# Performance work log

Hardware: AMD Instinct MI355X
Metric: run time of the kernel (lower is better)

Reference implementation:

```python
import jax, jax.numpy as jnp
import numpy as np

D_MODEL = 2048
HEADS = 16
HEAD_DIM = D_MODEL // HEADS
INNER = 8192
SEQ = 2048
EPS = 1e-5


def _layernorm(x, g, b):
    mu = jnp.mean(x, axis=-1, keepdims=True)
    var = jnp.mean(jnp.square(x - mu), axis=-1, keepdims=True)
    return (x - mu) * jax.lax.rsqrt(var + EPS) * g + b


def setup_inputs() -> dict:
    key = jax.random.key(0)
    ks = jax.random.split(key, 10)
    s = 0.02
    return {
        "x": jax.random.normal(ks[0], (1, SEQ, D_MODEL), dtype=jnp.float32),
        "C_w": jax.random.normal(ks[1], (D_MODEL, 3 * D_MODEL), dtype=jnp.float32) * s,
        "C_b": jnp.zeros((3 * D_MODEL,), dtype=jnp.float32),
        "lin_w": jax.random.normal(ks[2], (D_MODEL, D_MODEL), dtype=jnp.float32) * s,
        "lin_b": jnp.zeros((D_MODEL,), dtype=jnp.float32),
        "ff1_w": jax.random.normal(ks[3], (D_MODEL, INNER), dtype=jnp.float32) * s,
        "ff1_b": jnp.zeros((INNER,), dtype=jnp.float32),
        "ff2_w": jax.random.normal(ks[4], (INNER, D_MODEL), dtype=jnp.float32) * s,
        "ff2_b": jnp.zeros((D_MODEL,), dtype=jnp.float32),
        "ln1_g": jnp.ones((D_MODEL,), dtype=jnp.float32),
        "ln1_b": jnp.zeros((D_MODEL,), dtype=jnp.float32),
        "ln2_g": jnp.ones((D_MODEL,), dtype=jnp.float32),
        "ln2_b": jnp.zeros((D_MODEL,), dtype=jnp.float32),
    }


def reference(x, C_w, C_b, lin_w, lin_b, ff1_w, ff1_b, ff2_w, ff2_b,
              ln1_g, ln1_b, ln2_g, ln2_b):
    b, s, d = x.shape
    c = x @ C_w + C_b                       # [b, s, 3d]
    q, k, v = jnp.split(c, 3, axis=2)
    q = q.reshape(b, s, HEADS, HEAD_DIM)
    k = k.reshape(b, s, HEADS, HEAD_DIM)
    v = v.reshape(b, s, HEADS, HEAD_DIM)
    # NOTE: source scales by sqrt(d_model), NOT sqrt(head_dim)
    qk = jnp.einsum('bqhd,bkhd->bhqk', q, k) / jnp.sqrt(jnp.float32(d))
    causal = jnp.tril(jnp.ones((s, s), dtype=bool))  # [s, s]
    qk = jnp.where(causal[None, None, :, :], qk, -jnp.inf)
    scores = jax.nn.softmax(qk, axis=3)
    out = jnp.einsum('bhqk,bkhd->bqhd', scores, v).reshape(b, s, d)
    attn = out @ lin_w + lin_b
    h1 = _layernorm(x + attn, ln1_g, ln1_b)
    ff = jax.nn.gelu(h1 @ ff1_w + ff1_b, approximate=False) @ ff2_w + ff2_b
    return _layernorm(h1 + ff, ln2_g, ln2_b)
```

## Files before the change

kernel.cpp:

```cpp
#include <hip/hip_runtime.h>
#include <hip/hip_bf16.h>

#define SEQ 2048
#define DM 2048
#define NH 16
#define HD 128
#define FF 8192

typedef float f4v __attribute__((ext_vector_type(4)));
typedef short s8v __attribute__((ext_vector_type(8)));

__device__ __forceinline__ ushort f2bf(float f) {
  unsigned int x = __float_as_uint(f);
  unsigned int r = (x + 0x7FFFu + ((x >> 16) & 1u)) >> 16;
  return (ushort)r;
}

#define AS1 __attribute__((address_space(1)))
#define AS3 __attribute__((address_space(3)))
__device__ __forceinline__ void load16_lds(const ushort* g, ushort* l) {
  __builtin_amdgcn_global_load_lds((const AS1 unsigned int*)g, (AS3 unsigned int*)l, 16, 0, 0);
}

__global__ __launch_bounds__(256) void k_cvt(const float* __restrict__ in,
                                             ushort* __restrict__ out, int n4) {
  int i = blockIdx.x * 256 + threadIdx.x;
  if (i >= n4) return;
  f4v v = reinterpret_cast<const f4v*>(in)[i];
  ushort4 u;
  u.x = f2bf(v[0]); u.y = f2bf(v[1]); u.z = f2bf(v[2]); u.w = f2bf(v[3]);
  reinterpret_cast<ushort4*>(out)[i] = u;
}

__global__ __launch_bounds__(256) void k_tr(const float* __restrict__ W,
                                            ushort* __restrict__ Wt,
                                            int K, int N) {
  __shared__ float tile[32][36];
  int t = threadIdx.x;
  int n0 = blockIdx.x * 32, k0 = blockIdx.y * 32;
  int lr = t >> 3, lc = (t & 7) * 4;
  *(f4v*)&tile[lr][lc] = *(const f4v*)&W[(size_t)(k0 + lr) * N + n0 + lc];
  __syncthreads();
  int sn = t >> 3, sk = (t & 7) * 4;
  ushort4 u;
  u.x = f2bf(tile[sk + 0][sn]);
  u.y = f2bf(tile[sk + 1][sn]);
  u.z = f2bf(tile[sk + 2][sn]);
  u.w = f2bf(tile[sk + 3][sn]);
  *(ushort4*)&Wt[(size_t)(n0 + sn) * K + k0 + sk] = u;
}

#define GBM 256
#define GBN 256
#define GBK 32
#define TILE_SH (GBM * GBK)

__global__ __launch_bounds__(512, 2) void k_gemm256(
    const ushort* __restrict__ A, const ushort* __restrict__ Bt,
    const float* __restrict__ bias, float* __restrict__ Cf,
    ushort* __restrict__ Cb, int M, int N, int K, int gelu) {
  __shared__ ushort As[4 * TILE_SH];
  __shared__ ushort Bs[4 * TILE_SH];
  const int m0 = blockIdx.y * GBM, n0 = blockIdx.x * GBN;
  const int t = threadIdx.x;
  const int w = t >> 6, lane = t & 63;
  const int quad = lane >> 4, l16 = lane & 15;
  const int wm = (w >> 2) * 128, wn = (w & 3) * 64;
  const int kchunk = K / gridDim.z;
  const int kbeg = blockIdx.z * kchunk;
  const int NT = kchunk / GBK;
  if (Cf && gridDim.z > 1) Cf += (size_t)blockIdx.z * M * N;

  const int srow = lane >> 2;
  const int cg = (lane & 3) ^ ((srow >> 1) & 3);
  const ushort* gA = A + (size_t)(m0 + w * 32 + srow) * K + kbeg + cg * 8;
  const ushort* gB = Bt + (size_t)(n0 + w * 32 + srow) * K + kbeg + cg * 8;
  const int swz = (quad ^ ((l16 >> 1) & 3)) * 8;
  const int baseA = (wm + l16) * GBK + swz;
  const int baseB = (wn + l16) * GBK + swz;

  f4v acc[8][4] = {};

#pragma unroll
  for (int pt = 0; pt < 3; ++pt) {
    ushort* lA = &As[pt * TILE_SH + (w * 32) * GBK];
    ushort* lB = &Bs[pt * TILE_SH + (w * 32) * GBK];
    load16_lds(gA + pt * GBK, lA);
    load16_lds(gA + pt * GBK + (size_t)16 * K, lA + 16 * GBK);
    load16_lds(gB + pt * GBK, lB);
    load16_lds(gB + pt * GBK + (size_t)16 * K, lB + 16 * GBK);
  }
  asm volatile("s_waitcnt vmcnt(8)\n\ts_barrier" ::: "memory");

  for (int tt = 0; tt < NT; ++tt) {
    const ushort* At = &As[(tt & 3) * TILE_SH];
    const ushort* Bc = &Bs[(tt & 3) * TILE_SH];
    const int nb = (tt + 3) & 3;
    s8v a[8], b0, b1;
#pragma unroll
    for (int i = 0; i < 8; ++i)
      a[i] = *(const s8v*)&At[baseA + i * 16 * GBK];
    b0 = *(const s8v*)&Bc[baseB + 0 * 16 * GBK];
    b1 = *(const s8v*)&Bc[baseB + 1 * 16 * GBK];
    if (tt + 3 < NT) {
      ushort* lA = &As[nb * TILE_SH + (w * 32) * GBK];
      load16_lds(gA + (size_t)(tt + 3) * GBK, lA);
      load16_lds(gA + (size_t)(tt + 3) * GBK + (size_t)16 * K, lA + 16 * GBK);
    }
    __builtin_amdgcn_s_setprio(1);
#pragma unroll
    for (int i = 0; i < 8; ++i) {
      acc[i][0] = __builtin_amdgcn_mfma_f32_16x16x32_bf16(a[i], b0, acc[i][0], 0, 0, 0);
      acc[i][1] = __builtin_amdgcn_mfma_f32_16x16x32_bf16(a[i], b1, acc[i][1], 0, 0, 0);
    }
    __builtin_amdgcn_s_setprio(0);
    asm volatile("s_barrier" ::: "memory");
    s8v b2 = *(const s8v*)&Bc[baseB + 2 * 16 * GBK];
    s8v b3 = *(const s8v*)&Bc[baseB + 3 * 16 * GBK];
    if (tt + 3 < NT) {
      ushort* lB = &Bs[nb * TILE_SH + (w * 32) * GBK];
      load16_lds(gB + (size_t)(tt + 3) * GBK, lB);
      load16_lds(gB + (size_t)(tt + 3) * GBK + (size_t)16 * K, lB + 16 * GBK);
    }
    __builtin_amdgcn_s_setprio(1);
#pragma unroll
    for (int i = 0; i < 8; ++i) {
      acc[i][2] = __builtin_amdgcn_mfma_f32_16x16x32_bf16(a[i], b2, acc[i][2], 0, 0, 0);
      acc[i][3] = __builtin_amdgcn_mfma_f32_16x16x32_bf16(a[i], b3, acc[i][3], 0, 0, 0);
    }
    __builtin_amdgcn_s_setprio(0);
    if (tt + 4 <= NT) {
      asm volatile("s_waitcnt vmcnt(8)\n\ts_barrier" ::: "memory");
    } else if (tt + 3 <= NT) {
      asm volatile("s_waitcnt vmcnt(4)\n\ts_barrier" ::: "memory");
    } else if (tt + 2 <= NT) {
      asm volatile("s_waitcnt vmcnt(0)\n\ts_barrier" ::: "memory");
    }
  }

#pragma unroll
  for (int i = 0; i < 8; ++i) {
    int rbase = m0 + wm + i * 16 + quad * 4;
#pragma unroll
    for (int j = 0; j < 4; ++j) {
      int cidx = n0 + wn + j * 16 + l16;
      float b = bias ? bias[cidx] : 0.0f;
#pragma unroll
      for (int r = 0; r < 4; ++r) {
        float v = acc[i][j][r] + b;
        if (gelu) v = 0.5f * v * (1.0f + erff(v * 0.70710678118654752f));
        if (Cf) Cf[(size_t)(rbase + r) * N + cidx] = v;
        if (Cb) Cb[(size_t)(rbase + r) * N + cidx] = f2bf(v);
      }
    }
  }
}

__global__ __launch_bounds__(256) void k_attn_mfma(const ushort* __restrict__ qkv,
                                                   ushort* __restrict__ ctx) {
  __shared__ ushort Ks[64][136];
  __shared__ ushort Vt[128][72];
  __shared__ ushort Ps[4][16][72];
  const int idx = blockIdx.x;
  const int h = idx & (NH - 1);
  const int qt = (SEQ / 64 - 1) - (idx >> 4);
  const int q0 = qt * 64;
  const int t = threadIdx.x;
  const int wave = t >> 6, lane = t & 63;
  const int quad = lane >> 4, l16 = lane & 15;
  const float scale = 0.022097086912079608f;

  s8v aq[4];
  {
    const ushort* qp = qkv + (size_t)(q0 + 16 * wave + l16) * (3 * DM) + h * HD + quad * 8;
#pragma unroll
    for (int ks = 0; ks < 4; ++ks)
      aq[ks] = *(const s8v*)(qp + ks * 32);
  }
  f4v acc_o[8] = {};
  float m_r[4], l_r[4];
#pragma unroll
  for (int r = 0; r < 4; ++r) { m_r[r] = -1e30f; l_r[r] = 0.0f; }

  for (int kt = 0; kt <= qt; ++kt) {
    const int k0 = kt * 64;
    __syncthreads();
    {
      const ushort* kp = qkv + (size_t)k0 * (3 * DM) + DM + h * HD;
#pragma unroll
      for (int i = 0; i < 4; ++i) {
        int ch = t + i * 256;
        int row = ch >> 4, c8 = (ch & 15) * 8;
        *(s8v*)&Ks[row][c8] = *(const s8v*)(kp + (size_t)row * (3 * DM) + c8);
      }
      const ushort* vp = qkv + (size_t)k0 * (3 * DM) + 2 * DM + h * HD;
#pragma unroll
      for (int i = 0; i < 4; ++i) {
        int id = t + i * 256;
        int d = id & 127, sg = id >> 7;
        ushort e0 = vp[(size_t)(sg * 8 + 0) * (3 * DM) + d];
        ushort e1 = vp[(size_t)(sg * 8 + 1) * (3 * DM) + d];
        ushort e2 = vp[(size_t)(sg * 8 + 2) * (3 * DM) + d];
        ushort e3 = vp[(size_t)(sg * 8 + 3) * (3 * DM) + d];
        ushort e4 = vp[(size_t)(sg * 8 + 4) * (3 * DM) + d];
        ushort e5 = vp[(size_t)(sg * 8 + 5) * (3 * DM) + d];
        ushort e6 = vp[(size_t)(sg * 8 + 6) * (3 * DM) + d];
        ushort e7 = vp[(size_t)(sg * 8 + 7) * (3 * DM) + d];
        uint4 pk;
        pk.x = (uint)e0 | ((uint)e1 << 16);
        pk.y = (uint)e2 | ((uint)e3 << 16);
        pk.z = (uint)e4 | ((uint)e5 << 16);
        pk.w = (uint)e6 | ((uint)e7 << 16);
        *(uint4*)&Vt[d][sg * 8] = pk;
      }
    }
    __syncthreads();

    f4v sacc[4] = {};
#pragma unroll
    for (int ks = 0; ks < 4; ++ks) {
      s8v bk[4];
#pragma unroll
      for (int j = 0; j < 4; ++j)
        bk[j] = *(const s8v*)&Ks[j * 16 + l16][ks * 32 + quad * 8];
#pragma unroll
      for (int j = 0; j < 4; ++j)
        sacc[j] = __builtin_amdgcn_mfma_f32_16x16x32_bf16(aq[ks], bk[j], sacc[j], 0, 0, 0);
    }
    if (kt == qt) {
#pragma unroll
      for (int j = 0; j < 4; ++j)
#pragma unroll
        for (int r = 0; r < 4; ++r) {
          int lrow = 16 * wave + quad * 4 + r;
          int lcol = j * 16 + l16;
          sacc[j][r] = (lcol > lrow) ? -1e30f : sacc[j][r] * scale;
        }
    } else {
#pragma unroll
      for (int j = 0; j < 4; ++j)
#pragma unroll
        for (int r = 0; r < 4; ++r) sacc[j][r] *= scale;
    }
    float alpha[4];
#pragma unroll
    for (int r = 0; r < 4; ++r) {
      float mx = fmaxf(fmaxf(sacc[0][r], sacc[1][r]), fmaxf(sacc[2][r], sacc[3][r]));
      mx = fmaxf(mx, __shfl_xor(mx, 1));
      mx = fmaxf(mx, __shfl_xor(mx, 2));
      mx = fmaxf(mx, __shfl_xor(mx, 4));
      mx = fmaxf(mx, __shfl_xor(mx, 8));
      float mn = fmaxf(m_r[r], mx);
      alpha[r] = __expf(m_r[r] - mn);
      m_r[r] = mn;
      float ps = 0.0f;
#pragma unroll
      for (int j = 0; j < 4; ++j) {
        float p = __expf(sacc[j][r] - mn);
        sacc[j][r] = p;
        ps += p;
      }
      ps += __shfl_xor(ps, 1);
      ps += __shfl_xor(ps, 2);
      ps += __shfl_xor(ps, 4);
      ps += __shfl_xor(ps, 8);
      l_r[r] = l_r[r] * alpha[r] + ps;
    }
#pragma unroll
    for (int j = 0; j < 4; ++j)
#pragma unroll
      for (int r = 0; r < 4; ++r)
        Ps[wave][quad * 4 + r][j * 16 + l16] = f2bf(sacc[j][r]);
#pragma unroll
    for (int nd = 0; nd < 8; ++nd)
#pragma unroll
      for (int r = 0; r < 4; ++r) acc_o[nd][r] *= alpha[r];
#pragma unroll
    for (int ks2 = 0; ks2 < 2; ++ks2) {
      s8v ap = *(const s8v*)&Ps[wave][l16][ks2 * 32 + quad * 8];
#pragma unroll
      for (int nd = 0; nd < 8; ++nd) {
        s8v bv = *(const s8v*)&Vt[nd * 16 + l16][ks2 * 32 + quad * 8];
        acc_o[nd] = __builtin_amdgcn_mfma_f32_16x16x32_bf16(ap, bv, acc_o[nd], 0, 0, 0);
      }
    }
  }
  float rl[4];
#pragma unroll
  for (int r = 0; r < 4; ++r) rl[r] = 1.0f / l_r[r];
#pragma unroll
  for (int nd = 0; nd < 8; ++nd) {
    int col = h * HD + nd * 16 + l16;
#pragma unroll
    for (int r = 0; r < 4; ++r) {
      int row = q0 + 16 * wave + quad * 4 + r;
      ctx[(size_t)row * DM + col] = f2bf(acc_o[nd][r] * rl[r]);
    }
  }
}

__global__ __launch_bounds__(256) void k_ln_sk(const float* __restrict__ A,
                                               const float* __restrict__ P, int np,
                                               const float* __restrict__ bias,
                                               const float* __restrict__ g,
                                               const float* __restrict__ be,
                                               float* __restrict__ outf,
                                               ushort* __restrict__ outb) {
  int row = blockIdx.x;
  int t = threadIdx.x;
  const f4v* av = reinterpret_cast<const f4v*>(A + (size_t)row * DM);
  f4v x0 = av[t];
  f4v x1 = av[t + 256];
  for (int s = 0; s < np; ++s) {
    const f4v* pv = reinterpret_cast<const f4v*>(P + (size_t)s * SEQ * DM + (size_t)row * DM);
    x0 += pv[t];
    x1 += pv[t + 256];
  }
  const f4v* bb = reinterpret_cast<const f4v*>(bias);
  x0 += bb[t];
  x1 += bb[t + 256];
  float s = x0[0] + x0[1] + x0[2] + x0[3] + x1[0] + x1[1] + x1[2] + x1[3];
  float q = x0[0]*x0[0] + x0[1]*x0[1] + x0[2]*x0[2] + x0[3]*x0[3]
          + x1[0]*x1[0] + x1[1]*x1[1] + x1[2]*x1[2] + x1[3]*x1[3];
#pragma unroll
  for (int off = 32; off; off >>= 1) {
    s += __shfl_down(s, off, 64);
    q += __shfl_down(q, off, 64);
  }
  __shared__ float rs[4], rq[4];
  if ((t & 63) == 0) { rs[t >> 6] = s; rq[t >> 6] = q; }
  __syncthreads();
  s = rs[0] + rs[1] + rs[2] + rs[3];
  q = rq[0] + rq[1] + rq[2] + rq[3];
  float mu = s * (1.0f / DM);
  float var = q * (1.0f / DM) - mu * mu;
  float rstd = rsqrtf(var + 1e-5f);
  const f4v* gv = reinterpret_cast<const f4v*>(g);
  const f4v* bev = reinterpret_cast<const f4v*>(be);
  f4v y0 = (x0 - mu) * rstd * gv[t] + bev[t];
  f4v y1 = (x1 - mu) * rstd * gv[t + 256] + bev[t + 256];
  reinterpret_cast<f4v*>(outf + (size_t)row * DM)[t] = y0;
  reinterpret_cast<f4v*>(outf + (size_t)row * DM)[t + 256] = y1;
  if (outb) {
    ushort4 u0, u1;
    u0.x = f2bf(y0[0]); u0.y = f2bf(y0[1]); u0.z = f2bf(y0[2]); u0.w = f2bf(y0[3]);
    u1.x = f2bf(y1[0]); u1.y = f2bf(y1[1]); u1.z = f2bf(y1[2]); u1.w = f2bf(y1[3]);
    reinterpret_cast<ushort4*>(outb + (size_t)row * DM)[t] = u0;
    reinterpret_cast<ushort4*>(outb + (size_t)row * DM)[t + 256] = u1;
  }
}

extern "C" void kernel_launch(void* const* d_in, const int* in_sizes, int n_in,
                              void* d_out, int out_size, void* d_ws, size_t ws_size,
                              hipStream_t stream) {
  const float* x     = (const float*)d_in[0];
  const float* C_w   = (const float*)d_in[1];
  const float* C_b   = (const float*)d_in[2];
  const float* lin_w = (const float*)d_in[3];
  const float* lin_b = (const float*)d_in[4];
  const float* ff1_w = (const float*)d_in[5];
  const float* ff1_b = (const float*)d_in[6];
  const float* ff2_w = (const float*)d_in[7];
  const float* ff2_b = (const float*)d_in[8];
  const float* ln1g  = (const float*)d_in[9];
  const float* ln1b  = (const float*)d_in[10];
  const float* ln2g  = (const float*)d_in[11];
  const float* ln2b  = (const float*)d_in[12];

  char* ws = (char*)d_ws;
  size_t off = 0;
  auto take = [&](size_t bytes) {
    char* p = ws + off;
    off += (bytes + 255) & ~(size_t)255;
    return p;
  };
  ushort* Wt   = (ushort*)take((size_t)FF * DM * 2);
  ushort* qkvb = (ushort*)take((size_t)SEQ * 3 * DM * 2);
  ushort* xb   = (ushort*)take((size_t)SEQ * DM * 2);
  ushort* ctxb = (ushort*)take((size_t)SEQ * DM * 2);
  ushort* bigb = (ushort*)take((size_t)SEQ * FF * 2);
  float*  h1   = (float*) take((size_t)SEQ * DM * 4);
  float*  part = (float*) take((size_t)4 * SEQ * DM * 4);

  k_cvt<<<SEQ * DM / 1024, 256, 0, stream>>>(x, xb, SEQ * DM / 4);
  k_tr<<<dim3(3 * DM / 32, DM / 32), 256, 0, stream>>>(C_w, Wt, DM, 3 * DM);
  k_gemm256<<<dim3(3 * DM / 256, SEQ / 256, 1), 512, 0, stream>>>(xb, Wt, C_b, nullptr, qkvb, SEQ, 3 * DM, DM, 0);
  k_attn_mfma<<<dim3((SEQ / 64) * NH), 256, 0, stream>>>(qkvb, ctxb);
  k_tr<<<dim3(DM / 32, DM / 32), 256, 0, stream>>>(lin_w, Wt, DM, DM);
  k_gemm256<<<dim3(DM / 256, SEQ / 256, 4), 512, 0, stream>>>(ctxb, Wt, nullptr, part, nullptr, SEQ, DM, DM, 0);
  k_ln_sk<<<SEQ, 256, 0, stream>>>(x, part, 4, lin_b, ln1g, ln1b, h1, xb);
  k_tr<<<dim3(FF / 32, DM / 32), 256, 0, stream>>>(ff1_w, Wt, DM, FF);
  k_gemm256<<<dim3(FF / 256, SEQ / 256, 1), 512, 0, stream>>>(xb, Wt, ff1_b, nullptr, bigb, SEQ, FF, DM, 1);
  k_tr<<<dim3(DM / 32, FF / 32), 256, 0, stream>>>(ff2_w, Wt, FF, DM);
  k_gemm256<<<dim3(DM / 256, SEQ / 256, 4), 512, 0, stream>>>(bigb, Wt, nullptr, part, nullptr, SEQ, DM, FF, 0);
  k_ln_sk<<<SEQ, 256, 0, stream>>>(h1, part, 4, ff2_b, ln2g, ln2b, (float*)d_out, (ushort*)nullptr);
}
```

Measured before the change: 609.1 us.

## Split GEMM loop into four phases with register-prefetched LDS fragments

Restructures the bf16 MFMA GEMM main loop into four quarter-tile phases. While the current tile's MFMAs run, the A and B fragments for the next phase, and for the next k-tile, are loaded from LDS into registers. The global-to-LDS loads and their wait-count handling are interleaved across the phases. The aim is to hide LDS read latency behind matrix-core work. In exchange it doubles the number of barriers per iteration and adds more fragment registers, which could reduce occupancy or add synchronisation stalls.

```diff
diff --git a/kernel.cpp b/kernel.cpp
--- a/kernel.cpp
+++ b/kernel.cpp
@@ -21,6 +21,8 @@
 __device__ __forceinline__ void load16_lds(const ushort* g, ushort* l) {
   __builtin_amdgcn_global_load_lds((const AS1 unsigned int*)g, (AS3 unsigned int*)l, 16, 0, 0);
 }
+
+#define MFMA16(a, b, c) __builtin_amdgcn_mfma_f32_16x16x32_bf16((a), (b), (c), 0, 0, 0)
 
 __global__ __launch_bounds__(256) void k_cvt(const float* __restrict__ in,
                                              ushort* __restrict__ out, int n4) {
@@ -80,6 +82,7 @@
   const int baseB = (wn + l16) * GBK + swz;
 
   f4v acc[8][4] = {};
+  s8v A0[4], A1[4], B01[2], B23[2];
 
 #pragma unroll
   for (int pt = 0; pt < 3; ++pt) {
@@ -90,52 +93,82 @@
     load16_lds(gB + pt * GBK, lB);
     load16_lds(gB + pt * GBK + (size_t)16 * K, lB + 16 * GBK);
   }
-  asm volatile("s_waitcnt vmcnt(8)\n\ts_barrier" ::: "memory");
+  asm volatile("s_waitcnt vmcnt(8)" ::: "memory");
+  asm volatile("s_barrier" ::: "memory");
+#pragma unroll
+  for (int i = 0; i < 4; ++i) A0[i] = *(const s8v*)&As[baseA + i * 16 * GBK];
+  B01[0] = *(const s8v*)&Bs[baseB + 0 * 16 * GBK];
+  B01[1] = *(const s8v*)&Bs[baseB + 1 * 16 * GBK];
 
   for (int tt = 0; tt < NT; ++tt) {
-    const ushort* At = &As[(tt & 3) * TILE_SH];
-    const ushort* Bc = &Bs[(tt & 3) * TILE_SH];
-    const int nb = (tt + 3) & 3;
-    s8v a[8], b0, b1;
-#pragma unroll
-    for (int i = 0; i < 8; ++i)
-      a[i] = *(const s8v*)&At[baseA + i * 16 * GBK];
-    b0 = *(const s8v*)&Bc[baseB + 0 * 16 * GBK];
-    b1 = *(const s8v*)&Bc[baseB + 1 * 16 * GBK];
-    if (tt + 3 < NT) {
-      ushort* lA = &As[nb * TILE_SH + (w * 32) * GBK];
-      load16_lds(gA + (size_t)(tt + 3) * GBK, lA);
-      load16_lds(gA + (size_t)(tt + 3) * GBK + (size_t)16 * K, lA + 16 * GBK);
-    }
+    const ushort* Atc = &As[(tt & 3) * TILE_SH];
+    const ushort* Btc = &Bs[(tt & 3) * TILE_SH];
+    const ushort* Atn = &As[((tt + 1) & 3) * TILE_SH];
+    const ushort* Btn = &Bs[((tt + 1) & 3) * TILE_SH];
+    ushort* sA = &As[((tt + 3) & 3) * TILE_SH + (w * 32) * GBK];
+    ushort* sB = &Bs[((tt + 3) & 3) * TILE_SH + (w * 32) * GBK];
+    const bool st = (tt + 3 < NT), nx = (tt + 1 < NT);
+
+    B23[0] = *(const s8v*)&Btc[baseB + 2 * 16 * GBK];
+    B23[1] = *(const s8v*)&Btc[baseB + 3 * 16 * GBK];
+    if (st) {
+      load16_lds(gA + (size_t)(tt + 3) * GBK, sA);
+      load16_lds(gA + (size_t)(tt + 3) * GBK + (size_t)16 * K, sA + 16 * GBK);
+    }
+    asm volatile("s_barrier" ::: "memory");
     __builtin_amdgcn_s_setprio(1);
 #pragma unroll
-    for (int i = 0; i < 8; ++i) {
-      acc[i][0] = __builtin_amdgcn_mfma_f32_16x16x32_bf16(a[i], b0, acc[i][0], 0, 0, 0);
-      acc[i][1] = __builtin_amdgcn_mfma_f32_16x16x32_bf16(a[i], b1, acc[i][1], 0, 0, 0);
+    for (int i = 0; i < 4; ++i) {
+      acc[i][0] = MFMA16(A0[i], B01[0], acc[i][0]);
+      acc[i][1] = MFMA16(A0[i], B01[1], acc[i][1]);
     }
     __builtin_amdgcn_s_setprio(0);
+
+#pragma unroll
+    for (int i = 0; i < 4; ++i) A1[i] = *(const s8v*)&Atc[baseA + (i + 4) * 16 * GBK];
+    if (st) {
+      load16_lds(gB + (size_t)(tt + 3) * GBK, sB);
+      load16_lds(gB + (size_t)(tt + 3) * GBK + (size_t)16 * K, sB + 16 * GBK);
+      asm volatile("s_waitcnt vmcnt(8)" ::: "memory");
+    } else if (tt + 2 < NT) {
+      asm volatile("s_waitcnt vmcnt(4)" ::: "memory");
+    } else if (tt + 1 < NT) {
+      asm volatile("s_waitcnt vmcnt(0)" ::: "memory");
+    }
     asm volatile("s_barrier" ::: "memory");
-    s8v b2 = *(const s8v*)&Bc[baseB + 2 * 16 * GBK];
-    s8v b3 = *(const s8v*)&Bc[baseB + 3 * 16 * GBK];
-    if (tt + 3 < NT) {
-      ushort* lB = &Bs[nb * TILE_SH + (w * 32) * GBK];
-      load16_lds(gB + (size_t)(tt + 3) * GBK, lB);
-      load16_lds(gB + (size_t)(tt + 3) * GBK + (size_t)16 * K, lB + 16 * GBK);
-    }
     __builtin_amdgcn_s_setprio(1);
 #pragma unroll
-    for (int i = 0; i < 8; ++i) {
-      acc[i][2] = __builtin_amdgcn_mfma_f32_16x16x32_bf16(a[i], b2, acc[i][2], 0, 0, 0);
-      acc[i][3] = __builtin_amdgcn_mfma_f32_16x16x32_bf16(a[i], b3, acc[i][3], 0, 0, 0);
+    for (int i = 0; i < 4; ++i) {
+      acc[i][2] = MFMA16(A0[i], B23[0], acc[i][2]);
+      acc[i][3] = MFMA16(A0[i], B23[1], acc[i][3]);
     }
     __builtin_amdgcn_s_setprio(0);
-    if (tt + 4 <= NT) {
-      asm volatile("s_waitcnt vmcnt(8)\n\ts_barrier" ::: "memory");
-    } else if (tt + 3 <= NT) {
-      asm volatile("s_waitcnt vmcnt(4)\n\ts_barrier" ::: "memory");
-    } else if (tt + 2 <= NT) {
-      asm volatile("s_waitcnt vmcnt(0)\n\ts_barrier" ::: "memory");
-    }
+
+    if (nx) {
+#pragma unroll
+      for (int i = 0; i < 4; ++i) A0[i] = *(const s8v*)&Atn[baseA + i * 16 * GBK];
+    }
+    asm volatile("s_barrier" ::: "memory");
+    __builtin_amdgcn_s_setprio(1);
+#pragma unroll
+    for (int i = 0; i < 4; ++i) {
+      acc[i + 4][0] = MFMA16(A1[i], B01[0], acc[i + 4][0]);
+      acc[i + 4][1] = MFMA16(A1[i], B01[1], acc[i + 4][1]);
+    }
+    __builtin_amdgcn_s_setprio(0);
+
+    if (nx) {
+      B01[0] = *(const s8v*)&Btn[baseB + 0 * 16 * GBK];
+      B01[1] = *(const s8v*)&Btn[baseB + 1 * 16 * GBK];
+    }
+    asm volatile("s_barrier" ::: "memory");
+    __builtin_amdgcn_s_setprio(1);
+#pragma unroll
+    for (int i = 0; i < 4; ++i) {
+      acc[i + 4][2] = MFMA16(A1[i], B23[0], acc[i + 4][2]);
+      acc[i + 4][3] = MFMA16(A1[i], B23[1], acc[i + 4][3]);
+    }
+    __builtin_amdgcn_s_setprio(0);
   }
 
 #pragma unroll
```

Measured after the change: 631.5 us. +3.7%, slower.

## Restructure GEMM main loop with register double-buffered fragments and split-phase LDS reads

Applied to the files above, without the earlier changes.

Rewrites the GEMM inner loop so the A and B fragments for the next K-tile are read from LDS into a second register set while the current tile's MFMAs run. The loop is unrolled by two so the two B register sets can swap roles each step. It also splits the A fragment into two halves so half of the MFMAs can start before all of A is loaded, and changes the vmcnt wait and barrier placement to match. This is meant to hide LDS read latency behind matrix math, at the cost of more registers and stricter assumptions about buffer reuse (NT must be even).

```diff
diff --git a/kernel.cpp b/kernel.cpp
--- a/kernel.cpp
+++ b/kernel.cpp
@@ -21,6 +21,8 @@
 __device__ __forceinline__ void load16_lds(const ushort* g, ushort* l) {
   __builtin_amdgcn_global_load_lds((const AS1 unsigned int*)g, (AS3 unsigned int*)l, 16, 0, 0);
 }
+
+#define MFMA16(a, b, c) __builtin_amdgcn_mfma_f32_16x16x32_bf16((a), (b), (c), 0, 0, 0)
 
 __global__ __launch_bounds__(256) void k_cvt(const float* __restrict__ in,
                                              ushort* __restrict__ out, int n4) {
@@ -80,6 +82,7 @@
   const int baseB = (wn + l16) * GBK + swz;
 
   f4v acc[8][4] = {};
+  s8v A03[4], A47[4], BA[4], BB[4];
 
 #pragma unroll
   for (int pt = 0; pt < 3; ++pt) {
@@ -90,53 +93,66 @@
     load16_lds(gB + pt * GBK, lB);
     load16_lds(gB + pt * GBK + (size_t)16 * K, lB + 16 * GBK);
   }
-  asm volatile("s_waitcnt vmcnt(8)\n\ts_barrier" ::: "memory");
-
-  for (int tt = 0; tt < NT; ++tt) {
-    const ushort* At = &As[(tt & 3) * TILE_SH];
-    const ushort* Bc = &Bs[(tt & 3) * TILE_SH];
-    const int nb = (tt + 3) & 3;
-    s8v a[8], b0, b1;
-#pragma unroll
-    for (int i = 0; i < 8; ++i)
-      a[i] = *(const s8v*)&At[baseA + i * 16 * GBK];
-    b0 = *(const s8v*)&Bc[baseB + 0 * 16 * GBK];
-    b1 = *(const s8v*)&Bc[baseB + 1 * 16 * GBK];
-    if (tt + 3 < NT) {
-      ushort* lA = &As[nb * TILE_SH + (w * 32) * GBK];
-      load16_lds(gA + (size_t)(tt + 3) * GBK, lA);
-      load16_lds(gA + (size_t)(tt + 3) * GBK + (size_t)16 * K, lA + 16 * GBK);
-    }
-    __builtin_amdgcn_s_setprio(1);
-#pragma unroll
-    for (int i = 0; i < 8; ++i) {
-      acc[i][0] = __builtin_amdgcn_mfma_f32_16x16x32_bf16(a[i], b0, acc[i][0], 0, 0, 0);
-      acc[i][1] = __builtin_amdgcn_mfma_f32_16x16x32_bf16(a[i], b1, acc[i][1], 0, 0, 0);
-    }
-    __builtin_amdgcn_s_setprio(0);
-    asm volatile("s_barrier" ::: "memory");
-    s8v b2 = *(const s8v*)&Bc[baseB + 2 * 16 * GBK];
-    s8v b3 = *(const s8v*)&Bc[baseB + 3 * 16 * GBK];
-    if (tt + 3 < NT) {
-      ushort* lB = &Bs[nb * TILE_SH + (w * 32) * GBK];
-      load16_lds(gB + (size_t)(tt + 3) * GBK, lB);
-      load16_lds(gB + (size_t)(tt + 3) * GBK + (size_t)16 * K, lB + 16 * GBK);
-    }
-    __builtin_amdgcn_s_setprio(1);
-#pragma unroll
-    for (int i = 0; i < 8; ++i) {
-      acc[i][2] = __builtin_amdgcn_mfma_f32_16x16x32_bf16(a[i], b2, acc[i][2], 0, 0, 0);
-      acc[i][3] = __builtin_amdgcn_mfma_f32_16x16x32_bf16(a[i], b3, acc[i][3], 0, 0, 0);
-    }
-    __builtin_amdgcn_s_setprio(0);
-    if (tt + 4 <= NT) {
-      asm volatile("s_waitcnt vmcnt(8)\n\ts_barrier" ::: "memory");
-    } else if (tt + 3 <= NT) {
-      asm volatile("s_waitcnt vmcnt(4)\n\ts_barrier" ::: "memory");
-    } else if (tt + 2 <= NT) {
-      asm volatile("s_waitcnt vmcnt(0)\n\ts_barrier" ::: "memory");
-    }
-  }
+  asm volatile("s_waitcnt vmcnt(8)" ::: "memory");
+  asm volatile("s_barrier" ::: "memory");
+#pragma unroll
+  for (int i = 0; i < 4; ++i) A03[i] = *(const s8v*)&As[baseA + i * 16 * GBK];
+#pragma unroll
+  for (int j = 0; j < 4; ++j) BA[j] = *(const s8v*)&Bs[baseB + j * 16 * GBK];
+
+#define TILE_BODY(T, BUFC, BUFN, BC, BN)                                        \
+  {                                                                             \
+    const ushort* Atc = &As[(BUFC)*TILE_SH];                                    \
+         \
+    _Pragma("unroll") for (int i = 0; i < 4; ++i)                               \
+        A47[i] = *(const s8v*)&Atc[baseA + (i + 4) * 16 * GBK];                 \
+    if ((T) + 3 < NT) {                                                         \
+      ushort* sA = &As[(((T) + 3) & 3) * TILE_SH + (w * 32) * GBK];             \
+      load16_lds(gA + (size_t)((T) + 3) * GBK, sA);                             \
+      load16_lds(gA + (size_t)((T) + 3) * GBK + (size_t)16 * K, sA + 16 * GBK); \
+    }                                                                           \
+    __builtin_amdgcn_s_setprio(1);                                              \
+    _Pragma("unroll") for (int i = 0; i < 4; ++i)                               \
+        _Pragma("unroll") for (int j = 0; j < 4; ++j)                           \
+            acc[i][j] = MFMA16(A03[i], BC[j], acc[i][j]);                       \
+    __builtin_amdgcn_s_setprio(0);                                              \
+    if ((T) + 3 < NT)                                                           \
+      asm volatile("s_waitcnt vmcnt(6)" ::: "memory");                          \
+    else if ((T) + 2 < NT)                                                      \
+      asm volatile("s_waitcnt vmcnt(4)" ::: "memory");                          \
+    else                                                                        \
+      asm volatile("s_waitcnt vmcnt(0)" ::: "memory");                          \
+    asm volatile("s_barrier" ::: "memory");                                     \
+              \
+    if ((T) + 1 < NT) {                                                         \
+      const ushort* Atn = &As[(BUFN)*TILE_SH];                                  \
+      const ushort* Btn = &Bs[(BUFN)*TILE_SH];                                  \
+      _Pragma("unroll") for (int i = 0; i < 4; ++i)                             \
+          A03[i] = *(const s8v*)&Atn[baseA + i * 16 * GBK];                     \
+      _Pragma("unroll") for (int j = 0; j < 4; ++j)                             \
+          BN[j] = *(const s8v*)&Btn[baseB + j * 16 * GBK];                      \
+    }                                                                           \
+    if ((T) + 3 < NT) {                                                         \
+      ushort* sB = &Bs[(((T) + 3) & 3) * TILE_SH + (w * 32) * GBK];             \
+      load16_lds(gB + (size_t)((T) + 3) * GBK, sB);                             \
+      load16_lds(gB + (size_t)((T) + 3) * GBK + (size_t)16 * K, sB + 16 * GBK); \
+    }                                                                           \
+    __builtin_amdgcn_s_setprio(1);                                              \
+    _Pragma("unroll") for (int i = 0; i < 4; ++i)                               \
+        _Pragma("unroll") for (int j = 0; j < 4; ++j)                           \
+            acc[i + 4][j] = MFMA16(A47[i], BC[j], acc[i + 4][j]);               \
+    __builtin_amdgcn_s_setprio(0);                                              \
+    asm volatile("s_barrier" ::: "memory");                                     \
+  }
+
+  for (int tt = 0; tt < NT; tt += 2) {
+    const int b0 = tt & 3;
+    const int b1 = b0 + 1;
+    const int b2 = b0 ^ 2;
+    TILE_BODY(tt, b0, b1, BA, BB);
+    TILE_BODY(tt + 1, b1, b2, BB, BA);
+  }
+#undef TILE_BODY
 
 #pragma unroll
   for (int i = 0; i < 8; ++i) {
```

Result: no change. 612.2 us (+0.5%).
